# Optimization experiments

Hardware: AMD Instinct MI355X
Metric: run time of the kernel (lower is better)

## Reference

```python
import jax, jax.numpy as jnp
import numpy as np

SRC, B, SNT, E, C, V, EXT = 512, 16, 512, 512, 512, 12000, 500


def setup_inputs() -> dict:
    key = jax.random.key(0)
    ks = jax.random.split(key, 12)
    alignment_weight = jax.random.uniform(ks[0], (SRC, B, SNT), dtype=jnp.float32)
    arc_weight = jax.random.uniform(ks[1], (SRC, B, SRC), dtype=jnp.float32)
    rel_weight = jnp.zeros((1,), jnp.float32)
    concept_outs = jax.random.normal(ks[2], (SRC, B, E), dtype=jnp.float32)
    copy_seq = jax.random.randint(ks[3], (SNT, B, 2), 0, V + EXT)
    # pin the max so tot_ext = V + EXT is deterministic (torch uses copy_seq.max().item())
    copy_seq = copy_seq.at[0, 0, 0].set(V + EXT - 1)
    target = jax.random.randint(ks[4], (SRC, B), 0, V)
    target_rel = jnp.zeros((1,), jnp.int64 if jax.config.read('jax_enable_x64') else jnp.int32)
    std = 0.02
    W_transfer = jax.random.normal(ks[5], (C, E), jnp.float32) * std
    b_transfer = jnp.zeros((C,), jnp.float32)
    W_gen = jax.random.normal(ks[6], (V, C), jnp.float32) * std
    b_gen = jnp.zeros((V,), jnp.float32)
    W_div = jax.random.normal(ks[7], (3, C), jnp.float32) * std
    b_div = jnp.zeros((3,), jnp.float32)
    return dict(alignment_weight=alignment_weight, arc_weight=arc_weight,
                rel_weight=rel_weight, concept_outs=concept_outs,
                copy_seq=copy_seq, target=target, target_rel=target_rel,
                bsz=B, src_len=SRC,
                W_transfer=W_transfer, b_transfer=b_transfer,
                W_gen=W_gen, b_gen=b_gen, W_div=W_div, b_div=b_div)


def reference(alignment_weight, arc_weight, rel_weight, concept_outs, copy_seq,
              target, target_rel, bsz, src_len,
              W_transfer, b_transfer, W_gen, b_gen, W_div, b_div):
    # work=True inference path of ArcConceptDecoder (joint_rel=False, separate_rel=False)
    snt_len = alignment_weight.shape[-1]
    copy_seq = copy_seq[:snt_len]                       # [snt, B, 2]
    h = jnp.tanh(concept_outs @ W_transfer.T + b_transfer)  # [src, B, C]
    gates = jax.nn.softmax(h @ W_div.T + b_div, axis=-1)     # [src, B, 3]
    gen_gate = gates[..., 0:1]
    map_gate = gates[..., 1:2]
    copy_gate = gates[..., 2:3]
    copy_gate2 = jnp.concatenate([copy_gate, map_gate], axis=-1)  # [src, B, 2]
    probs = gen_gate * jax.nn.softmax(h @ W_gen.T + b_gen, axis=-1)  # [src, B, V]
    vocab = probs.shape[-1]
    tot_ext = vocab + EXT
    probs = jnp.concatenate(
        [probs, jnp.zeros(probs.shape[:-1] + (tot_ext - vocab,), probs.dtype)], axis=-1)
    # index: copy_seq.transpose(0,1).view(1,B,-1).expand(src,-1,-1)
    index = jnp.transpose(copy_seq, (1, 0, 2)).reshape(1, probs.shape[1], -1)  # [1, B, snt*2]
    index = jnp.broadcast_to(index, (probs.shape[0],) + index.shape[1:])       # [src, B, snt*2]
    copy_probs = (copy_gate2[:, :, None, :] * alignment_weight[..., None])
    copy_probs = copy_probs.reshape(probs.shape[0], probs.shape[1], -1)        # [src, B, snt*2]
    # scatter_add along last dim
    S, Bv = probs.shape[0], probs.shape[1]
    flat_probs = probs.reshape(S * Bv, tot_ext)
    flat_idx = index.reshape(S * Bv, -1)
    flat_cp = copy_probs.reshape(S * Bv, -1)
    rows = jnp.arange(S * Bv)[:, None]
    flat_probs = flat_probs.at[rows, flat_idx].add(flat_cp)
    probs = flat_probs.reshape(S, Bv, tot_ext)
    ll = jnp.log(probs + 1e-12)
    arc_ll = jnp.log(arc_weight + 1e-12)
    return ll, arc_ll
```

## Files before the change

### kernel.cpp

```cpp
#include <hip/hip_runtime.h>
#include <hip/hip_bf16.h>

#define SRCL 512
#define BSZ  16
#define SNTL 512
#define CDIM 512
#define KDIM 512
#define VOC  12000
#define EXTN 500
#define MROWS (SRCL*BSZ)
#define TOTV (VOC+EXTN)
#define NPAD 12032
#define LL_SIZE ((size_t)MROWS * TOTV)

typedef __attribute__((ext_vector_type(8))) short bf16x8;
typedef __attribute__((ext_vector_type(4))) float f32x4;

__device__ __forceinline__ unsigned short f2bf(float x) {
  union { __hip_bfloat16 b; unsigned short u; } c;
  c.b = __float2bfloat16(x);
  return c.u;
}
__device__ __forceinline__ float bflo(unsigned int u) { return __uint_as_float(u << 16); }
__device__ __forceinline__ float bfhi(unsigned int u) { return __uint_as_float(u & 0xffff0000u); }

__device__ __forceinline__ void gload16(const void* g, void* l) {
  __builtin_amdgcn_global_load_lds(
      (const __attribute__((address_space(1))) unsigned int*)g,
      (__attribute__((address_space(3))) unsigned int*)l, 16, 0, 0);
}

__device__ __forceinline__ float wred_max(float v) {
  for (int o = 32; o; o >>= 1) v = fmaxf(v, __shfl_down(v, o, 64));
  return v;
}
__device__ __forceinline__ float wred_sum(float v) {
  for (int o = 32; o; o >>= 1) v += __shfl_down(v, o, 64);
  return v;
}

__global__ void cvt_kernel(const float* __restrict__ co, const float* __restrict__ wt,
                           const float* __restrict__ wg,
                           unsigned short* __restrict__ cob,
                           unsigned short* __restrict__ wtb,
                           unsigned short* __restrict__ wgb) {
  const int stride = gridDim.x * blockDim.x;
  const int t0 = blockIdx.x * blockDim.x + threadIdx.x;
  for (int i = t0; i < MROWS*KDIM/4; i += stride) {
    const float4 v = ((const float4*)co)[i];
    ushort4 o; o.x = f2bf(v.x); o.y = f2bf(v.y); o.z = f2bf(v.z); o.w = f2bf(v.w);
    ((ushort4*)cob)[i] = o;
  }
  for (int i = t0; i < CDIM*KDIM/4; i += stride) {
    const float4 v = ((const float4*)wt)[i];
    ushort4 o; o.x = f2bf(v.x); o.y = f2bf(v.y); o.z = f2bf(v.z); o.w = f2bf(v.w);
    ((ushort4*)wtb)[i] = o;
  }
  for (int i = t0; i < NPAD*KDIM/4; i += stride) {
    float4 v = make_float4(0.f, 0.f, 0.f, 0.f);
    if (i < VOC*KDIM/4) v = ((const float4*)wg)[i];
    ushort4 o; o.x = f2bf(v.x); o.y = f2bf(v.y); o.z = f2bf(v.z); o.w = f2bf(v.w);
    ((ushort4*)wgb)[i] = o;
  }
}

template<int EPI>
__launch_bounds__(256)
__global__ void gemm_bt(const short* __restrict__ A, const short* __restrict__ Bm,
                        const float* __restrict__ bias, void* __restrict__ outp) {
  __shared__ short As[128*64];
  __shared__ short Bs[128*64];
  const int tid  = threadIdx.x;
  const int wave = tid >> 6;
  const int lane = tid & 63;

  const int nwg = gridDim.x * gridDim.y;
  int bid = blockIdx.y * gridDim.x + blockIdx.x;
  bid = (bid & 7) * (nwg >> 3) + (bid >> 3);
  const int bx = bid % gridDim.x;
  const int by = bid / gridDim.x;
  const int m0 = by * 128;
  const int n0 = bx * 128;

  const int srow = lane >> 3;
  const int ssk  = ((lane & 7) ^ srow) * 8;
  const size_t aBase = (size_t)(m0 + wave*32 + srow) * KDIM + ssk;
  const size_t bBase = (size_t)(n0 + wave*32 + srow) * KDIM + ssk;
  short* lA = As + wave*32*64;
  short* lB = Bs + wave*32*64;

  const int wm = wave & 1, wn = wave >> 1;
  const int quad = lane >> 4, r16 = lane & 15;
  const int rsw  = r16 & 7;
  const int aoffb = (wm*64 + r16) * 64;
  const int boffb = (wn*64 + r16) * 64;

  f32x4 acc[4][4];
#pragma unroll
  for (int i = 0; i < 4; ++i)
#pragma unroll
    for (int j = 0; j < 4; ++j) acc[i][j] = (f32x4){0.f,0.f,0.f,0.f};

  for (int kt = 0; kt < KDIM/64; ++kt) {
    const size_t ko = (size_t)kt * 64;
    __syncthreads();
#pragma unroll
    for (int j = 0; j < 4; ++j) {
      gload16(A  + aBase + ko + (size_t)j*8*KDIM, lA + j*512);
      gload16(Bm + bBase + ko + (size_t)j*8*KDIM, lB + j*512);
    }
    __syncthreads();
#pragma unroll
    for (int ks = 0; ks < 2; ++ks) {
      const int kc = ((ks*4 + quad) ^ rsw) * 8;
      bf16x8 af[4], bf[4];
#pragma unroll
      for (int i = 0; i < 4; ++i) {
        af[i] = *(const bf16x8*)(As + aoffb + i*1024 + kc);
        bf[i] = *(const bf16x8*)(Bs + boffb + i*1024 + kc);
      }
#pragma unroll
      for (int mi = 0; mi < 4; ++mi)
#pragma unroll
        for (int ni = 0; ni < 4; ++ni)
          acc[mi][ni] = __builtin_amdgcn_mfma_f32_16x16x32_bf16(af[mi], bf[ni], acc[mi][ni], 0, 0, 0);
    }
  }

#pragma unroll
  for (int mi = 0; mi < 4; ++mi) {
#pragma unroll
    for (int ni = 0; ni < 4; ++ni) {
#pragma unroll
      for (int r = 0; r < 4; ++r) {
        const int row = m0 + wm*64 + mi*16 + quad*4 + r;
        const int col = n0 + wn*64 + ni*16 + r16;
        float v = acc[mi][ni][r];
        if constexpr (EPI == 0) {
          v = tanhf(v + bias[col]);
          ((unsigned short*)outp)[(size_t)row * CDIM + col] = f2bf(v);
        } else if constexpr (EPI == 1) {
          v += (col < VOC) ? bias[col] : 0.f;
          ((float*)outp)[(size_t)row * TOTV + col] = v;
        } else {
          v += (col < VOC) ? bias[col] : 0.f;
          ((unsigned short*)outp)[(size_t)row * NPAD + col] = f2bf(v);
        }
      }
    }
  }
}

template<int BF16L>
__launch_bounds__(1024)
__global__ void finalize_kernel(const void* __restrict__ lg, float* __restrict__ out,
                                const __hip_bfloat16* __restrict__ hmat,
                                const float* __restrict__ Wd, const float* __restrict__ bd,
                                const int* __restrict__ copy_seq,
                                const float* __restrict__ align) {
  __shared__ __align__(16) float p[TOTV];
  __shared__ float scr[16];
  __shared__ float gscr[24];
  __shared__ float gv[3];
  const int m = blockIdx.x;
  const int b = m & 15;
  const int tid = threadIdx.x;
  float* row = out + (size_t)m * TOTV;

  {
    float d0 = 0.f, d1 = 0.f, d2 = 0.f;
    if (tid < CDIM) {
      const float hv = __bfloat162float(hmat[(size_t)m*CDIM + tid]);
      d0 = hv * Wd[tid];
      d1 = hv * Wd[CDIM + tid];
      d2 = hv * Wd[2*CDIM + tid];
    }
    d0 = wred_sum(d0); d1 = wred_sum(d1); d2 = wred_sum(d2);
    const int w = tid >> 6;
    if ((tid & 63) == 0 && w < 8) { gscr[w*3] = d0; gscr[w*3+1] = d1; gscr[w*3+2] = d2; }
  }
  __syncthreads();
  if (tid == 0) {
    float g0 = bd[0], g1 = bd[1], g2 = bd[2];
    for (int i = 0; i < 8; ++i) { g0 += gscr[i*3]; g1 += gscr[i*3+1]; g2 += gscr[i*3+2]; }
    const float mg = fmaxf(g0, fmaxf(g1, g2));
    const float e0 = __expf(g0-mg), e1 = __expf(g1-mg), e2 = __expf(g2-mg);
    const float inv3 = 1.f / (e0 + e1 + e2);
    gv[0] = e0*inv3; gv[1] = e1*inv3; gv[2] = e2*inv3;
  }

  float mx = -1e30f;
  if constexpr (BF16L) {
    const uint4* rowv = (const uint4*)((const unsigned short*)lg + (size_t)m * NPAD);
    for (int i = tid; i < VOC/8; i += 1024) {
      const uint4 q = rowv[i];
      float4 lo, hi;
      lo.x = bflo(q.x); lo.y = bfhi(q.x); lo.z = bflo(q.y); lo.w = bfhi(q.y);
      hi.x = bflo(q.z); hi.y = bfhi(q.z); hi.z = bflo(q.w); hi.w = bfhi(q.w);
      ((float4*)p)[i*2]   = lo;
      ((float4*)p)[i*2+1] = hi;
      mx = fmaxf(mx, fmaxf(fmaxf(fmaxf(lo.x,lo.y),fmaxf(lo.z,lo.w)),
                           fmaxf(fmaxf(hi.x,hi.y),fmaxf(hi.z,hi.w))));
    }
  } else {
    const float4* rowv = (const float4*)row;
    for (int i = tid; i < VOC/4; i += 1024) {
      const float4 v = rowv[i];
      ((float4*)p)[i] = v;
      mx = fmaxf(mx, fmaxf(fmaxf(v.x, v.y), fmaxf(v.z, v.w)));
    }
  }
  for (int i = VOC + tid; i < TOTV; i += 1024) p[i] = 0.f;

  mx = wred_max(mx);
  if ((tid & 63) == 0) scr[tid >> 6] = mx;
  __syncthreads();
  mx = scr[0];
#pragma unroll
  for (int i = 1; i < 16; ++i) mx = fmaxf(mx, scr[i]);
  __syncthreads();

  float sm = 0.f;
  for (int i = tid; i < VOC; i += 1024) {
    const float e = __expf(p[i] - mx);
    p[i] = e;
    sm += e;
  }
  sm = wred_sum(sm);
  if ((tid & 63) == 0) scr[tid >> 6] = sm;
  __syncthreads();
  sm = scr[0];
#pragma unroll
  for (int i = 1; i < 16; ++i) sm += scr[i];

  const float gen  = gv[0];
  const float mapg = gv[1];
  const float cpg  = gv[2];
  const float scale = gen / sm;
  const float inv   = sm / gen;
  const float cw = cpg * inv, mw = mapg * inv;

  if (tid < SNTL) {
    const float aw = align[(size_t)m * SNTL + tid];
    const int2 cs = *(const int2*)&copy_seq[(tid*BSZ + b)*2];
    atomicAdd(&p[cs.x], cw * aw);
    atomicAdd(&p[cs.y], mw * aw);
  }
  __syncthreads();

  for (int i = tid; i < TOTV/4; i += 1024) {
    const float4 v = ((const float4*)p)[i];
    float4 r;
    r.x = __logf(fmaf(v.x, scale, 1e-12f));
    r.y = __logf(fmaf(v.y, scale, 1e-12f));
    r.z = __logf(fmaf(v.z, scale, 1e-12f));
    r.w = __logf(fmaf(v.w, scale, 1e-12f));
    ((float4*)row)[i] = r;
  }
}

__global__ void arc_kernel(const float4* __restrict__ arc, float4* __restrict__ out) {
  const int i = blockIdx.x * blockDim.x + threadIdx.x;
  if (i < (SRCL*BSZ*SRCL)/4) {
    const float4 v = arc[i];
    float4 r;
    r.x = __logf(v.x + 1e-12f);
    r.y = __logf(v.y + 1e-12f);
    r.z = __logf(v.z + 1e-12f);
    r.w = __logf(v.w + 1e-12f);
    out[i] = r;
  }
}

extern "C" void kernel_launch(void* const* d_in, const int* in_sizes, int n_in,
                              void* d_out, int out_size, void* d_ws, size_t ws_size,
                              hipStream_t stream) {
  (void)in_sizes; (void)n_in; (void)out_size;
  const float* align   = (const float*)d_in[0];
  const float* arc     = (const float*)d_in[1];
  const float* concept = (const float*)d_in[3];
  const int*   cseq    = (const int*)d_in[4];
  const float* Wt = (const float*)d_in[9];
  const float* bt = (const float*)d_in[10];
  const float* Wg = (const float*)d_in[11];
  const float* bg = (const float*)d_in[12];
  const float* Wd = (const float*)d_in[13];
  const float* bd = (const float*)d_in[14];
  float* out = (float*)d_out;

  unsigned short* cob = (unsigned short*)d_ws;
  unsigned short* wtb = cob + (size_t)MROWS*KDIM;
  unsigned short* wgb = wtb + (size_t)CDIM*KDIM;
  unsigned short* hb  = wgb + (size_t)NPAD*KDIM;
  unsigned short* logitsb = hb + (size_t)MROWS*KDIM;
  const size_t need = (size_t)((char*)(logitsb + (size_t)MROWS*NPAD) - (char*)d_ws);
  const bool use_bf16_logits = (ws_size >= need);

  cvt_kernel<<<2048, 256, 0, stream>>>(concept, Wt, Wg, cob, wtb, wgb);
  gemm_bt<0><<<dim3(CDIM/128, MROWS/128), 256, 0, stream>>>(
      (const short*)cob, (const short*)wtb, bt, (void*)hb);
  if (use_bf16_logits) {
    gemm_bt<2><<<dim3(NPAD/128, MROWS/128), 256, 0, stream>>>(
        (const short*)hb, (const short*)wgb, bg, (void*)logitsb);
    finalize_kernel<1><<<MROWS, 1024, 0, stream>>>(
        logitsb, out, (const __hip_bfloat16*)hb, Wd, bd, cseq, align);
  } else {
    gemm_bt<1><<<dim3(NPAD/128, MROWS/128), 256, 0, stream>>>(
        (const short*)hb, (const short*)wgb, bg, (void*)out);
    finalize_kernel<0><<<MROWS, 1024, 0, stream>>>(
        out, out, (const __hip_bfloat16*)hb, Wd, bd, cseq, align);
  }
  arc_kernel<<<4096, 256, 0, stream>>>((const float4*)arc, (float4*)(out + LL_SIZE));
}
```

Baseline: 823.5 us.

## Keep softmax logits in registers and simplify GEMM to 32-wide K tiles

```diff
diff --git a/kernel.cpp b/kernel.cpp
--- a/kernel.cpp
+++ b/kernel.cpp
@@ -68,32 +68,27 @@
 __launch_bounds__(256)
 __global__ void gemm_bt(const short* __restrict__ A, const short* __restrict__ Bm,
                         const float* __restrict__ bias, void* __restrict__ outp) {
-  __shared__ short As[128*64];
-  __shared__ short Bs[128*64];
+  __shared__ short As[128*32];
+  __shared__ short Bs[128*32];
   const int tid  = threadIdx.x;
   const int wave = tid >> 6;
   const int lane = tid & 63;
-
-  const int nwg = gridDim.x * gridDim.y;
-  int bid = blockIdx.y * gridDim.x + blockIdx.x;
-  bid = (bid & 7) * (nwg >> 3) + (bid >> 3);
-  const int bx = bid % gridDim.x;
-  const int by = bid / gridDim.x;
-  const int m0 = by * 128;
-  const int n0 = bx * 128;
-
-  const int srow = lane >> 3;
-  const int ssk  = ((lane & 7) ^ srow) * 8;
-  const size_t aBase = (size_t)(m0 + wave*32 + srow) * KDIM + ssk;
-  const size_t bBase = (size_t)(n0 + wave*32 + srow) * KDIM + ssk;
-  short* lA = As + wave*32*64;
-  short* lB = Bs + wave*32*64;
+  const int m0 = blockIdx.y * 128;
+  const int n0 = blockIdx.x * 128;
+
+  const int lrow = lane >> 2;
+  const int lkof = (lane & 3) * 8;
+  const size_t aG0 = (size_t)(m0 + wave*32 + lrow) * KDIM + lkof;
+  const size_t aG1 = aG0 + (size_t)16 * KDIM;
+  const size_t bG0 = (size_t)(n0 + wave*32 + lrow) * KDIM + lkof;
+  const size_t bG1 = bG0 + (size_t)16 * KDIM;
+  short* lA0 = As + wave*1024;  short* lA1 = lA0 + 512;
+  short* lB0 = Bs + wave*1024;  short* lB1 = lB0 + 512;
 
   const int wm = wave & 1, wn = wave >> 1;
   const int quad = lane >> 4, r16 = lane & 15;
-  const int rsw  = r16 & 7;
-  const int aoffb = (wm*64 + r16) * 64;
-  const int boffb = (wn*64 + r16) * 64;
+  const int aoff = (wm*64 + r16)*32 + quad*8;
+  const int boff = (wn*64 + r16)*32 + quad*8;
 
   f32x4 acc[4][4];
 #pragma unroll
@@ -101,30 +96,25 @@
 #pragma unroll
     for (int j = 0; j < 4; ++j) acc[i][j] = (f32x4){0.f,0.f,0.f,0.f};
 
-  for (int kt = 0; kt < KDIM/64; ++kt) {
-    const size_t ko = (size_t)kt * 64;
+  for (int kt = 0; kt < KDIM/32; ++kt) {
+    const int kof = kt * 32;
     __syncthreads();
-#pragma unroll
-    for (int j = 0; j < 4; ++j) {
-      gload16(A  + aBase + ko + (size_t)j*8*KDIM, lA + j*512);
-      gload16(Bm + bBase + ko + (size_t)j*8*KDIM, lB + j*512);
-    }
+    gload16(A  + aG0 + kof, lA0);
+    gload16(A  + aG1 + kof, lA1);
+    gload16(Bm + bG0 + kof, lB0);
+    gload16(Bm + bG1 + kof, lB1);
     __syncthreads();
-#pragma unroll
-    for (int ks = 0; ks < 2; ++ks) {
-      const int kc = ((ks*4 + quad) ^ rsw) * 8;
-      bf16x8 af[4], bf[4];
-#pragma unroll
-      for (int i = 0; i < 4; ++i) {
-        af[i] = *(const bf16x8*)(As + aoffb + i*1024 + kc);
-        bf[i] = *(const bf16x8*)(Bs + boffb + i*1024 + kc);
-      }
-#pragma unroll
-      for (int mi = 0; mi < 4; ++mi)
-#pragma unroll
-        for (int ni = 0; ni < 4; ++ni)
-          acc[mi][ni] = __builtin_amdgcn_mfma_f32_16x16x32_bf16(af[mi], bf[ni], acc[mi][ni], 0, 0, 0);
-    }
+    bf16x8 af[4], bf[4];
+#pragma unroll
+    for (int i = 0; i < 4; ++i) {
+      af[i] = *(const bf16x8*)(As + aoff + i*512);
+      bf[i] = *(const bf16x8*)(Bs + boff + i*512);
+    }
+#pragma unroll
+    for (int mi = 0; mi < 4; ++mi)
+#pragma unroll
+      for (int ni = 0; ni < 4; ++ni)
+        acc[mi][ni] = __builtin_amdgcn_mfma_f32_16x16x32_bf16(af[mi], bf[ni], acc[mi][ni], 0, 0, 0);
   }
 
 #pragma unroll
@@ -160,12 +150,16 @@
                                 const float* __restrict__ align) {
   __shared__ __align__(16) float p[TOTV];
   __shared__ float scr[16];
+  __shared__ float scr2[16];
   __shared__ float gscr[24];
   __shared__ float gv[3];
   const int m = blockIdx.x;
   const int b = m & 15;
   const int tid = threadIdx.x;
   float* row = out + (size_t)m * TOTV;
+
+  for (int i = tid; i < TOTV/4; i += 1024)
+    ((float4*)p)[i] = make_float4(0.f, 0.f, 0.f, 0.f);
 
   {
     float d0 = 0.f, d1 = 0.f, d2 = 0.f;
@@ -179,7 +173,46 @@
     const int w = tid >> 6;
     if ((tid & 63) == 0 && w < 8) { gscr[w*3] = d0; gscr[w*3+1] = d1; gscr[w*3+2] = d2; }
   }
+
+  float v[16];
+  float mx = -1e30f;
+  bool hasB;
+  if constexpr (BF16L) {
+    const uint4* rowv = (const uint4*)((const unsigned short*)lg + (size_t)m * NPAD);
+    const uint4 q0 = rowv[tid];
+    v[0]=bflo(q0.x); v[1]=bfhi(q0.x); v[2]=bflo(q0.y); v[3]=bfhi(q0.y);
+    v[4]=bflo(q0.z); v[5]=bfhi(q0.z); v[6]=bflo(q0.w); v[7]=bfhi(q0.w);
+    hasB = tid < (VOC/8 - 1024);
+    if (hasB) {
+      const uint4 q1 = rowv[tid + 1024];
+      v[8]=bflo(q1.x);  v[9]=bfhi(q1.x);  v[10]=bflo(q1.y); v[11]=bfhi(q1.y);
+      v[12]=bflo(q1.z); v[13]=bfhi(q1.z); v[14]=bflo(q1.w); v[15]=bfhi(q1.w);
+#pragma unroll
+      for (int j = 8; j < 16; ++j) mx = fmaxf(mx, v[j]);
+    }
+#pragma unroll
+    for (int j = 0; j < 8; ++j) mx = fmaxf(mx, v[j]);
+  } else {
+    const float4* rowv = (const float4*)row;
+    const float4 f0 = rowv[tid];
+    const float4 f1 = rowv[tid + 1024];
+    v[0]=f0.x; v[1]=f0.y; v[2]=f0.z; v[3]=f0.w;
+    v[4]=f1.x; v[5]=f1.y; v[6]=f1.z; v[7]=f1.w;
+    hasB = tid < (VOC/4 - 2048);
+    if (hasB) {
+      const float4 f2 = rowv[tid + 2048];
+      v[8]=f2.x; v[9]=f2.y; v[10]=f2.z; v[11]=f2.w;
+#pragma unroll
+      for (int j = 8; j < 12; ++j) mx = fmaxf(mx, v[j]);
+    }
+#pragma unroll
+    for (int j = 0; j < 8; ++j) mx = fmaxf(mx, v[j]);
+  }
+
+  mx = wred_max(mx);
+  if ((tid & 63) == 0) scr[tid >> 6] = mx;
   __syncthreads();
+
   if (tid == 0) {
     float g0 = bd[0], g1 = bd[1], g2 = bd[2];
     for (int i = 0; i < 8; ++i) { g0 += gscr[i*3]; g1 += gscr[i*3+1]; g2 += gscr[i*3+2]; }
@@ -189,49 +222,28 @@
     gv[0] = e0*inv3; gv[1] = e1*inv3; gv[2] = e2*inv3;
   }
 
-  float mx = -1e30f;
-  if constexpr (BF16L) {
-    const uint4* rowv = (const uint4*)((const unsigned short*)lg + (size_t)m * NPAD);
-    for (int i = tid; i < VOC/8; i += 1024) {
-      const uint4 q = rowv[i];
-      float4 lo, hi;
-      lo.x = bflo(q.x); lo.y = bfhi(q.x); lo.z = bflo(q.y); lo.w = bfhi(q.y);
-      hi.x = bflo(q.z); hi.y = bfhi(q.z); hi.z = bflo(q.w); hi.w = bfhi(q.w);
-      ((float4*)p)[i*2]   = lo;
-      ((float4*)p)[i*2+1] = hi;
-      mx = fmaxf(mx, fmaxf(fmaxf(fmaxf(lo.x,lo.y),fmaxf(lo.z,lo.w)),
-                           fmaxf(fmaxf(hi.x,hi.y),fmaxf(hi.z,hi.w))));
-    }
-  } else {
-    const float4* rowv = (const float4*)row;
-    for (int i = tid; i < VOC/4; i += 1024) {
-      const float4 v = rowv[i];
-      ((float4*)p)[i] = v;
-      mx = fmaxf(mx, fmaxf(fmaxf(v.x, v.y), fmaxf(v.z, v.w)));
-    }
-  }
-  for (int i = VOC + tid; i < TOTV; i += 1024) p[i] = 0.f;
-
-  mx = wred_max(mx);
-  if ((tid & 63) == 0) scr[tid >> 6] = mx;
+  mx = scr[0];
+#pragma unroll
+  for (int i = 1; i < 16; ++i) mx = fmaxf(mx, scr[i]);
+
+  float sm = 0.f;
+#pragma unroll
+  for (int j = 0; j < 8; ++j) { v[j] = __expf(v[j] - mx); sm += v[j]; }
+  if (hasB) {
+    if constexpr (BF16L) {
+#pragma unroll
+      for (int j = 8; j < 16; ++j) { v[j] = __expf(v[j] - mx); sm += v[j]; }
+    } else {
+#pragma unroll
+      for (int j = 8; j < 12; ++j) { v[j] = __expf(v[j] - mx); sm += v[j]; }
+    }
+  }
+  sm = wred_sum(sm);
+  if ((tid & 63) == 0) scr2[tid >> 6] = sm;
   __syncthreads();
-  mx = scr[0];
-#pragma unroll
-  for (int i = 1; i < 16; ++i) mx = fmaxf(mx, scr[i]);
-  __syncthreads();
-
-  float sm = 0.f;
-  for (int i = tid; i < VOC; i += 1024) {
-    const float e = __expf(p[i] - mx);
-    p[i] = e;
-    sm += e;
-  }
-  sm = wred_sum(sm);
-  if ((tid & 63) == 0) scr[tid >> 6] = sm;
-  __syncthreads();
-  sm = scr[0];
-#pragma unroll
-  for (int i = 1; i < 16; ++i) sm += scr[i];
+  sm = scr2[0];
+#pragma unroll
+  for (int i = 1; i < 16; ++i) sm += scr2[i];
 
   const float gen  = gv[0];
   const float mapg = gv[1];
@@ -248,13 +260,61 @@
   }
   __syncthreads();
 
-  for (int i = tid; i < TOTV/4; i += 1024) {
-    const float4 v = ((const float4*)p)[i];
+  if constexpr (BF16L) {
+    {
+      const int c = tid;
+      const float4 d0 = ((const float4*)p)[2*c];
+      const float4 d1 = ((const float4*)p)[2*c + 1];
+      float4 r0, r1;
+      r0.x = __logf(fmaf(v[0] + d0.x, scale, 1e-12f));
+      r0.y = __logf(fmaf(v[1] + d0.y, scale, 1e-12f));
+      r0.z = __logf(fmaf(v[2] + d0.z, scale, 1e-12f));
+      r0.w = __logf(fmaf(v[3] + d0.w, scale, 1e-12f));
+      r1.x = __logf(fmaf(v[4] + d1.x, scale, 1e-12f));
+      r1.y = __logf(fmaf(v[5] + d1.y, scale, 1e-12f));
+      r1.z = __logf(fmaf(v[6] + d1.z, scale, 1e-12f));
+      r1.w = __logf(fmaf(v[7] + d1.w, scale, 1e-12f));
+      ((float4*)row)[2*c]   = r0;
+      ((float4*)row)[2*c+1] = r1;
+    }
+    if (hasB) {
+      const int c = tid + 1024;
+      const float4 d0 = ((const float4*)p)[2*c];
+      const float4 d1 = ((const float4*)p)[2*c + 1];
+      float4 r0, r1;
+      r0.x = __logf(fmaf(v[8]  + d0.x, scale, 1e-12f));
+      r0.y = __logf(fmaf(v[9]  + d0.y, scale, 1e-12f));
+      r0.z = __logf(fmaf(v[10] + d0.z, scale, 1e-12f));
+      r0.w = __logf(fmaf(v[11] + d0.w, scale, 1e-12f));
+      r1.x = __logf(fmaf(v[12] + d1.x, scale, 1e-12f));
+      r1.y = __logf(fmaf(v[13] + d1.y, scale, 1e-12f));
+      r1.z = __logf(fmaf(v[14] + d1.z, scale, 1e-12f));
+      r1.w = __logf(fmaf(v[15] + d1.w, scale, 1e-12f));
+      ((float4*)row)[2*c]   = r0;
+      ((float4*)row)[2*c+1] = r1;
+    }
+  } else {
+#pragma unroll
+    for (int cc = 0; cc < 3; ++cc) {
+      if (cc == 2 && !hasB) break;
+      const int c = tid + cc*1024;
+      const float4 d = ((const float4*)p)[c];
+      float4 r;
+      r.x = __logf(fmaf(v[cc*4+0] + d.x, scale, 1e-12f));
+      r.y = __logf(fmaf(v[cc*4+1] + d.y, scale, 1e-12f));
+      r.z = __logf(fmaf(v[cc*4+2] + d.z, scale, 1e-12f));
+      r.w = __logf(fmaf(v[cc*4+3] + d.w, scale, 1e-12f));
+      ((float4*)row)[c] = r;
+    }
+  }
+  if (tid < (TOTV - VOC)/4) {
+    const int i = VOC/4 + tid;
+    const float4 d = ((const float4*)p)[i];
     float4 r;
-    r.x = __logf(fmaf(v.x, scale, 1e-12f));
-    r.y = __logf(fmaf(v.y, scale, 1e-12f));
-    r.z = __logf(fmaf(v.z, scale, 1e-12f));
-    r.w = __logf(fmaf(v.w, scale, 1e-12f));
+    r.x = __logf(fmaf(d.x, scale, 1e-12f));
+    r.y = __logf(fmaf(d.y, scale, 1e-12f));
+    r.z = __logf(fmaf(d.z, scale, 1e-12f));
+    r.w = __logf(fmaf(d.w, scale, 1e-12f));
     ((float4*)row)[i] = r;
   }
 }
```

Measured after the change: 819.9 us. About the same (-0.4%).
